# Performance work log

Hardware: AMD Instinct MI355X
Metric: run time of the kernel (lower is better)

The kernel has to match this reference:

```python
import jax, jax.numpy as jnp
import numpy as np

N = 100000
E = 1600000
IN_DIM = 128
HID = 128
OUT_DIM = 64
ORDER = 4


def setup_inputs() -> dict:
    key = jax.random.key(0)
    ks = jax.random.split(key, 10)
    x = jax.random.normal(ks[0], (N, IN_DIM), dtype=jnp.float32)
    edge_index = jax.random.randint(ks[1], (2, E), 0, N, dtype=jnp.int64)
    gen_edge_index = jax.random.randint(ks[2], (2, E), 0, N, dtype=jnp.int64)
    s = 1.0 / np.sqrt(IN_DIM)
    w_orig = jax.random.normal(ks[3], (ORDER + 1, IN_DIM, HID), dtype=jnp.float32) * s
    b_orig = jax.random.normal(ks[4], (ORDER + 1, HID), dtype=jnp.float32) * s
    w_aug = jax.random.normal(ks[5], (ORDER + 1, IN_DIM, HID), dtype=jnp.float32) * s
    b_aug = jax.random.normal(ks[6], (ORDER + 1, HID), dtype=jnp.float32) * s
    fusion_weight = jnp.ones((2,), dtype=jnp.float32)
    clf_w = jax.random.normal(ks[7], (HID, OUT_DIM), dtype=jnp.float32) / np.sqrt(HID)
    clf_b = jax.random.normal(ks[8], (OUT_DIM,), dtype=jnp.float32) / np.sqrt(HID)
    return {"x": x, "edge_index": edge_index, "gen_edge_index": gen_edge_index,
            "w_orig": w_orig, "b_orig": b_orig, "w_aug": w_aug, "b_aug": b_aug,
            "fusion_weight": fusion_weight, "clf_w": clf_w, "clf_b": clf_b}


def _beta_wavelet(x, edge_index, W, b, num_nodes):
    # add self loops
    loop = jnp.arange(num_nodes, dtype=edge_index.dtype)
    row = jnp.concatenate([edge_index[0], loop])
    col = jnp.concatenate([edge_index[1], loop])
    # symmetric normalization D^{-1/2} A D^{-1/2}
    deg = jax.ops.segment_sum(jnp.ones_like(col, dtype=x.dtype), col, num_segments=num_nodes)
    dinv = jnp.where(deg > 0, deg ** -0.5, 0.0)
    norm = dinv[row] * dinv[col]  # [E+N]
    out = x @ W[0] + b[0]
    Tx = x
    for i in range(1, ORDER + 1):
        msg = norm[:, None] * Tx[row]                      # gather + scale [E+N, D]
        Tx = jax.ops.segment_sum(msg, col, num_segments=num_nodes)  # scatter_add
        out = out + Tx @ W[i] + b[i]
    return jax.nn.relu(out)


def reference(x, edge_index, gen_edge_index, w_orig, b_orig, w_aug, b_aug, fusion_weight, clf_w, clf_b):
    num_nodes = x.shape[0]
    h_orig = _beta_wavelet(x, edge_index, w_orig, b_orig, num_nodes)
    h_aug = _beta_wavelet(x, gen_edge_index, w_aug, b_aug, num_nodes)
    w = jax.nn.softmax(fusion_weight)
    h_final = w[0] * h_orig + w[1] * h_aug
    return h_final @ clf_w + clf_b
```

## Files before the change

### kernel.cpp

```cpp
#include <hip/hip_runtime.h>

#define N_NODES 100000
#define NPAD    100096
#define NE      1600000
#define DIM     128
#define ODIM    64
#define NORDER  4
#define KTOT    640
#define NB      391
#define PB_EDGES 16384
#define PB_BLKS  98

typedef _Float16 h8 __attribute__((ext_vector_type(8)));
typedef float f4 __attribute__((ext_vector_type(4)));

__device__ __forceinline__ float2 up2(unsigned p) {
    union { unsigned u; _Float16 h[2]; } c; c.u = p;
    return make_float2((float)c.h[0], (float)c.h[1]);
}
__device__ __forceinline__ unsigned pk2(float x, float y) {
    union { unsigned u; _Float16 h[2]; } c;
    c.h[0] = (_Float16)x; c.h[1] = (_Float16)y;
    return c.u;
}
__device__ __forceinline__ unsigned short f2hbits(float x) {
    union { _Float16 h; unsigned short s; } c;
    c.h = (_Float16)x;
    return c.s;
}
__device__ __forceinline__ float h2f(unsigned short s) {
    union { unsigned short u; _Float16 h; } c;
    c.u = s;
    return (float)c.h;
}
__device__ __forceinline__ void async_cp16(const void* g, void* l) {
    __builtin_amdgcn_global_load_lds((const __attribute__((address_space(1))) void*)g,
                                     (__attribute__((address_space(3))) void*)l, 16, 0, 0);
}

__global__ __launch_bounds__(256) void hist_edges(const int* __restrict__ e0,
                                                  const int* __restrict__ e1,
                                                  int* __restrict__ bhist) {
    __shared__ int lh[NB];
    int t = threadIdx.x;
    int g = blockIdx.x >= 782;
    int blk = g ? (blockIdx.x - 782) : blockIdx.x;
    const int* colp = (g ? e1 : e0) + NE;
    int* bh = bhist + g * NB;
    for (int i = t; i < NB; i += 256) lh[i] = 0;
    __syncthreads();
    int base = blk * 2048 + t;
#pragma unroll
    for (int j = 0; j < 8; ++j) {
        int e = base + j * 256;
        if (e < NE) atomicAdd(&lh[colp[e] >> 8], 1);
    }
    __syncthreads();
    for (int i = t; i < NB; i += 256) if (lh[i]) atomicAdd(&bh[i], lh[i]);
}

__global__ void wave_scan(const int* __restrict__ in,
                          int* __restrict__ oexcl,
                          int* __restrict__ ocur,
                          int n) {
    int wv = threadIdx.x >> 6, lane = threadIdx.x & 63;
    if (wv >= 2) return;
    const int* I = in + wv * n;
    int* O = oexcl + wv * (n + 1);
    int* C = ocur + wv * n;
    int carry = 0;
    for (int base = 0; base < n; base += 64) {
        int i = base + lane;
        int v = (i < n) ? I[i] : 0;
        int s = v;
#pragma unroll
        for (int off = 1; off < 64; off <<= 1) {
            int x = __shfl_up(s, off, 64);
            if (lane >= off) s += x;
        }
        int excl = carry + s - v;
        if (i < n) {
            O[i] = excl;
            C[i] = excl;
        }
        carry += __shfl(s, 63, 64);
    }
    if (lane == 0) O[n] = carry;
}

__global__ __launch_bounds__(1024) void part_edges(const int* __restrict__ e0,
                                                   const int* __restrict__ e1,
                                                   int* __restrict__ bcursor,
                                                   unsigned* __restrict__ pairs) {
    __shared__ int lh[NB];
    __shared__ int lpos[NB];
    int t = threadIdx.x;
    int g = blockIdx.x >= PB_BLKS;
    int blk = g ? (blockIdx.x - PB_BLKS) : blockIdx.x;
    const int* rowp = (g ? e1 : e0);
    const int* colp = rowp + NE;
    int* bc = bcursor + g * NB;
    unsigned* pr = pairs + (size_t)g * NE;
    for (int i = t; i < NB; i += 1024) lh[i] = 0;
    __syncthreads();
    int base = blk * PB_EDGES + t;
    int rank[16];
    short bk[16];
    unsigned char lcv[16];
#pragma unroll
    for (int j = 0; j < 16; ++j) {
        int e = base + j * 1024;
        rank[j] = -1;
        if (e < NE) {
            int c = colp[e];
            bk[j] = (short)(c >> 8);
            lcv[j] = (unsigned char)(c & 255);
            rank[j] = atomicAdd(&lh[c >> 8], 1);
        }
    }
    __syncthreads();
    for (int i = t; i < NB; i += 1024) {
        int n = lh[i];
        lpos[i] = n ? atomicAdd(&bc[i], n) : 0;
    }
    __syncthreads();
#pragma unroll
    for (int j = 0; j < 16; ++j) {
        int e = base + j * 1024;
        if (e < NE) {
            int b = bk[j];
            pr[lpos[b] + rank[j]] = ((unsigned)rowp[e] << 8) | lcv[j];
        }
    }
}

__global__ __launch_bounds__(256) void bucket_csr(const unsigned* __restrict__ pairs,
                                                  const int* __restrict__ boff,
                                                  int* __restrict__ ptrv,
                                                  float* __restrict__ dinv,
                                                  int* __restrict__ srcv) {
    __shared__ int lcnt[256];
    __shared__ int lbase[256];
    int t = threadIdx.x;
    int g = blockIdx.x >= NB;
    int b = g ? (blockIdx.x - NB) : blockIdx.x;
    const unsigned* pr = pairs + (size_t)g * NE;
    const int* bo = boff + g * (NB + 1);
    int* pv = ptrv + g * (N_NODES + 1);
    float* dv = dinv + g * N_NODES;
    int* sv = srcv + (size_t)g * NE;
    lcnt[t] = 0;
    __syncthreads();
    int s = bo[b], e = bo[b + 1];
    for (int i = s + t; i < e; i += 256)
        atomicAdd(&lcnt[pr[i] & 255u], 1);
    __syncthreads();
    int v = lcnt[t];
    lbase[t] = v;
    __syncthreads();
    for (int off = 1; off < 256; off <<= 1) {
        int x = (t >= off) ? lbase[t - off] : 0;
        __syncthreads();
        lbase[t] += x;
        __syncthreads();
    }
    int node = (b << 8) + t;
    int gbase = s + lbase[t] - v;
    lbase[t] = gbase;
    lcnt[t] = 0;
    if (node < N_NODES) {
        pv[node] = gbase;
        dv[node] = rsqrtf((float)(v + 1));
    }
    if (b == 0 && g == 0 && t == 0) ptrv[N_NODES] = NE;
    if (b == 0 && g == 1 && t == 0) ptrv[2 * N_NODES + 1] = NE;
    __syncthreads();
    for (int i = s + t; i < e; i += 256) {
        unsigned pk = pr[i];
        int lc = (int)(pk & 255u);
        int pos = lbase[lc] + atomicAdd(&lcnt[lc], 1);
        sv[pos] = (int)(pk >> 8);
    }
}

__global__ __launch_bounds__(256) void xcast(const float* __restrict__ x,
                                             unsigned* __restrict__ Tbig) {
    int idx = blockIdx.x * 256 + threadIdx.x;
    if (idx >= NPAD * 64) return;
    int m = idx >> 6, u = idx & 63;
    int e = (m << 7) + u * 2;
    float a = (m < N_NODES) ? x[e]     : 0.f;
    float b = (m < N_NODES) ? x[e + 1] : 0.f;
    Tbig[m * 320 + u] = pk2(a, b);
}

__global__ __launch_bounds__(256) void wcast(const float* __restrict__ Wo,
                                             const float* __restrict__ Wa,
                                             const float* __restrict__ cw,
                                             unsigned short* __restrict__ Wt) {
    int idx = blockIdx.x * 256 + threadIdx.x;
    if (idx >= 2 * 5 * DIM * DIM + ODIM * DIM) return;
    if (idx < 2 * 5 * DIM * DIM) {
        int g   = idx / (5 * DIM * DIM);
        int rem = idx % (5 * DIM * DIM);
        int i   = rem / (DIM * DIM);
        int r2  = rem % (DIM * DIM);
        int k8  = r2 >> 10;
        int n   = (r2 >> 3) & 127;
        int k7  = r2 & 7;
        int k   = k8 * 8 + k7;
        const float* W = g ? Wa : Wo;
        Wt[idx] = f2hbits(W[(i * DIM + k) * DIM + n]);
    } else {
        int j = idx - 2 * 5 * DIM * DIM;
        int n = j >> 7, k = j & 127;
        Wt[idx] = f2hbits(cw[k * ODIM + n]);
    }
}

__global__ __launch_bounds__(256) void propagate(const unsigned* __restrict__ Tin,
                                                 unsigned* __restrict__ Tout,
                                                 const int* __restrict__ ptrv,
                                                 const int* __restrict__ srcv,
                                                 const float* __restrict__ dinv) {
    int gid  = blockIdx.x * 256 + threadIdx.x;
    int lane = threadIdx.x & 63;
    int v    = __builtin_amdgcn_readfirstlane(gid >> 6);
    if (v >= N_NODES) return;
    float dv = dinv[v];
    float2 self = up2(Tin[v * 320 + lane]);
    float ax = dv * dv * self.x;
    float ay = dv * dv * self.y;
    int beg = ptrv[v], end = ptrv[v + 1];
    int k = beg;
    for (; k + 16 <= end; k += 16) {
        int u[16];
#pragma unroll
        for (int j = 0; j < 16; ++j) u[j] = srcv[k + j];
        float2 tt[16];
#pragma unroll
        for (int j = 0; j < 16; ++j) tt[j] = up2(Tin[u[j] * 320 + lane]);
        float w[16];
#pragma unroll
        for (int j = 0; j < 16; ++j) w[j] = dinv[u[j]] * dv;
#pragma unroll
        for (int j = 0; j < 16; ++j) { ax += w[j] * tt[j].x; ay += w[j] * tt[j].y; }
    }
    for (; k + 4 <= end; k += 4) {
        int u[4];
#pragma unroll
        for (int j = 0; j < 4; ++j) u[j] = srcv[k + j];
        float2 tt[4];
#pragma unroll
        for (int j = 0; j < 4; ++j) tt[j] = up2(Tin[u[j] * 320 + lane]);
        float w[4];
#pragma unroll
        for (int j = 0; j < 4; ++j) w[j] = dinv[u[j]] * dv;
#pragma unroll
        for (int j = 0; j < 4; ++j) { ax += w[j] * tt[j].x; ay += w[j] * tt[j].y; }
    }
    for (; k < end; ++k) {
        int u = srcv[k];
        float w = dinv[u] * dv;
        float2 t = up2(Tin[u * 320 + lane]);
        ax += w * t.x; ay += w * t.y;
    }
    Tout[v * 320 + lane] = pk2(ax, ay);
}

__global__ __launch_bounds__(256, 3) void gemmH0(
        const unsigned short* __restrict__ A,
        const unsigned short* __restrict__ Wt,
        const float* __restrict__ bO,
        const float* __restrict__ fw,
        unsigned short* __restrict__ H0) {
    __shared__ unsigned short Bl[DIM * DIM];
    __shared__ float bsl[DIM];
    int t = threadIdx.x;
    int lane = t & 63, wv = t >> 6;
    int m0 = blockIdx.x * 128 + wv * 32;
    int l15 = lane & 15, q = lane >> 4;
    if (t < 128) {
        float s = 0.f;
        for (int i = 0; i <= NORDER; ++i) s += bO[i * DIM + t];
        bsl[t] = s;
    }
    float f0 = fw[0], f1 = fw[1];
    float mx = fmaxf(f0, f1);
    float e0 = expf(f0 - mx), e1 = expf(f1 - mx);
    float sw0 = e0 / (e0 + e1);

    f4 acc[2][8];
#pragma unroll
    for (int mt = 0; mt < 2; ++mt)
#pragma unroll
        for (int nt = 0; nt < 8; ++nt) acc[mt][nt] = (f4)(0.f);

#pragma unroll
    for (int i = 0; i < 5; ++i) {
        const unsigned short* WtI = Wt + (size_t)i * DIM * DIM;
        h8 af[2][4];
#pragma unroll
        for (int mt = 0; mt < 2; ++mt)
#pragma unroll
            for (int kc = 0; kc < 4; ++kc)
                af[mt][kc] = *(const h8*)(A + (size_t)(m0 + mt * 16 + l15) * KTOT
                                            + i * DIM + (kc * 4 + q) * 8);
#pragma unroll
        for (int c = 0; c < 8; ++c) {
            int ci = c * 4 + wv;
            async_cp16(WtI + ci * 512 + lane * 8, &Bl[ci * 512]);
        }
        __syncthreads();
#pragma unroll
        for (int kc = 0; kc < 4; ++kc) {
            int c = kc * 4 + q;
#pragma unroll
            for (int nt = 0; nt < 8; ++nt) {
                h8 bf = *(const h8*)&Bl[(size_t)(c * 128 + nt * 16 + l15) * 8];
                acc[0][nt] = __builtin_amdgcn_mfma_f32_16x16x32_f16(af[0][kc], bf, acc[0][nt], 0, 0, 0);
                acc[1][nt] = __builtin_amdgcn_mfma_f32_16x16x32_f16(af[1][kc], bf, acc[1][nt], 0, 0, 0);
            }
        }
        __syncthreads();
    }
#pragma unroll
    for (int mt = 0; mt < 2; ++mt)
#pragma unroll
        for (int nt = 0; nt < 8; ++nt) {
            float bsv = bsl[nt * 16 + l15];
#pragma unroll
            for (int r = 0; r < 4; ++r) {
                int row = m0 + mt * 16 + q * 4 + r;
                H0[(size_t)row * DIM + nt * 16 + l15] =
                    f2hbits(sw0 * fmaxf(acc[mt][nt][r] + bsv, 0.f));
            }
        }
}

__global__ __launch_bounds__(256, 2) void gemm_fused2(
        const unsigned short* __restrict__ A,
        const unsigned short* __restrict__ Wt,
        const unsigned short* __restrict__ H0,
        const float* __restrict__ bA,
        const float* __restrict__ fw,
        const unsigned short* __restrict__ clfWt,
        const float* __restrict__ clfB,
        float* __restrict__ out) {
    __shared__ unsigned short BlH[DIM * 132];
    __shared__ float bsl[DIM];
    unsigned short* Bl = BlH;
    unsigned short* Hl = BlH;
    int t = threadIdx.x;
    int lane = t & 63, wv = t >> 6;
    int m0 = blockIdx.x * 128 + wv * 32;
    int l15 = lane & 15, q = lane >> 4;
    if (t < 128) {
        float s = 0.f;
        for (int i = 0; i <= NORDER; ++i) s += bA[i * DIM + t];
        bsl[t] = s;
    }
    float f0 = fw[0], f1 = fw[1];
    float mx = fmaxf(f0, f1);
    float e0 = expf(f0 - mx), e1 = expf(f1 - mx);
    float sw1 = e1 / (e0 + e1);

    f4 acc[2][8];
#pragma unroll
    for (int mt = 0; mt < 2; ++mt)
#pragma unroll
        for (int nt = 0; nt < 8; ++nt) acc[mt][nt] = (f4)(0.f);

#pragma unroll
    for (int i = 0; i < 5; ++i) {
        const unsigned short* WtI = Wt + (size_t)i * DIM * DIM;
        h8 af[2][4];
#pragma unroll
        for (int mt = 0; mt < 2; ++mt)
#pragma unroll
            for (int kc = 0; kc < 4; ++kc)
                af[mt][kc] = *(const h8*)(A + (size_t)(m0 + mt * 16 + l15) * KTOT
                                            + i * DIM + (kc * 4 + q) * 8);
#pragma unroll
        for (int c = 0; c < 8; ++c) {
            int ci = c * 4 + wv;
            async_cp16(WtI + ci * 512 + lane * 8, &Bl[ci * 512]);
        }
        __syncthreads();
#pragma unroll
        for (int kc = 0; kc < 4; ++kc) {
            int c = kc * 4 + q;
#pragma unroll
            for (int nt = 0; nt < 8; ++nt) {
                h8 bf = *(const h8*)&Bl[(size_t)(c * 128 + nt * 16 + l15) * 8];
                acc[0][nt] = __builtin_amdgcn_mfma_f32_16x16x32_f16(af[0][kc], bf, acc[0][nt], 0, 0, 0);
                acc[1][nt] = __builtin_amdgcn_mfma_f32_16x16x32_f16(af[1][kc], bf, acc[1][nt], 0, 0, 0);
            }
        }
        __syncthreads();
    }

#pragma unroll
    for (int mt = 0; mt < 2; ++mt)
#pragma unroll
        for (int nt = 0; nt < 8; ++nt) {
            float bsv = bsl[nt * 16 + l15];
            int col = nt * 16 + l15;
#pragma unroll
            for (int r = 0; r < 4; ++r) {
                int lrow = wv * 32 + mt * 16 + q * 4 + r;
                int grow = m0 + mt * 16 + q * 4 + r;
                float h = sw1 * fmaxf(acc[mt][nt][r] + bsv, 0.f)
                        + h2f(H0[(size_t)grow * DIM + col]);
                Hl[lrow * 132 + col] = f2hbits(h);
            }
        }
    __syncthreads();

    f4 o[2][4];
#pragma unroll
    for (int mt = 0; mt < 2; ++mt)
#pragma unroll
        for (int n2 = 0; n2 < 4; ++n2) o[mt][n2] = (f4)(0.f);
#pragma unroll
    for (int kc = 0; kc < 4; ++kc) {
        int c = kc * 4 + q;
        h8 ha[2];
#pragma unroll
        for (int mt = 0; mt < 2; ++mt)
            ha[mt] = *(const h8*)&Hl[(wv * 32 + mt * 16 + l15) * 132 + c * 8];
#pragma unroll
        for (int n2 = 0; n2 < 4; ++n2) {
            h8 bf = *(const h8*)&clfWt[(size_t)(n2 * 16 + l15) * DIM + c * 8];
            o[0][n2] = __builtin_amdgcn_mfma_f32_16x16x32_f16(ha[0], bf, o[0][n2], 0, 0, 0);
            o[1][n2] = __builtin_amdgcn_mfma_f32_16x16x32_f16(ha[1], bf, o[1][n2], 0, 0, 0);
        }
    }
#pragma unroll
    for (int mt = 0; mt < 2; ++mt)
#pragma unroll
        for (int n2 = 0; n2 < 4; ++n2) {
            int col = n2 * 16 + l15;
            float cbv = clfB[col];
#pragma unroll
            for (int r = 0; r < 4; ++r) {
                int row = m0 + mt * 16 + q * 4 + r;
                if (row < N_NODES) out[(size_t)row * ODIM + col] = o[mt][n2][r] + cbv;
            }
        }
}

extern "C" void kernel_launch(void* const* d_in, const int* in_sizes, int n_in,
                              void* d_out, int out_size, void* d_ws, size_t ws_size,
                              hipStream_t stream) {
    const float* x   = (const float*)d_in[0];
    const int*   ei  = (const int*)d_in[1];
    const int*   gi  = (const int*)d_in[2];
    const float* w_o = (const float*)d_in[3];
    const float* b_o = (const float*)d_in[4];
    const float* w_a = (const float*)d_in[5];
    const float* b_a = (const float*)d_in[6];
    const float* fw  = (const float*)d_in[7];
    const float* cw  = (const float*)d_in[8];
    const float* cb  = (const float*)d_in[9];
    float* out = (float*)d_out;

    char* p = (char*)d_ws;
    auto alloc = [&](size_t bytes) {
        void* r = (void*)p;
        p += (bytes + 255) & ~(size_t)255;
        return r;
    };
    unsigned* Tbig = (unsigned*)alloc((size_t)NPAD * 320 * 4);
    unsigned short* H0 = (unsigned short*)alloc((size_t)NPAD * DIM * 2);
    unsigned short* Wt = (unsigned short*)alloc(((size_t)2 * 5 * DIM * DIM + ODIM * DIM) * 2);
    float* dinv  = (float*)alloc((size_t)2 * N_NODES * 4);
    unsigned* pairs = (unsigned*)alloc((size_t)2 * NE * 4);
    int* csr_src = (int*)alloc((size_t)2 * NE * 4);
    int* csr_ptr = (int*)alloc((size_t)2 * (N_NODES + 1) * 4);
    int* bhist   = (int*)alloc((size_t)2 * NB * 4);
    int* boff    = (int*)alloc((size_t)2 * (NB + 1) * 4);
    int* bcursor = (int*)alloc((size_t)2 * NB * 4);

    const int gP  = (N_NODES * 64 + 255) / 256;
    const int gX  = (NPAD * 64 + 255) / 256;
    const int gW  = (2 * 5 * DIM * DIM + ODIM * DIM + 255) / 256;
    const int gM  = NPAD / 128;

    xcast<<<gX, 256, 0, stream>>>(x, Tbig);
    wcast<<<gW, 256, 0, stream>>>(w_o, w_a, cw, Wt);

    hipMemsetAsync(bhist, 0, (size_t)2 * NB * 4, stream);
    hist_edges<<<2 * 782, 256, 0, stream>>>(ei, gi, bhist);
    wave_scan<<<1, 128, 0, stream>>>(bhist, boff, bcursor, NB);
    part_edges<<<2 * PB_BLKS, 1024, 0, stream>>>(ei, gi, bcursor, pairs);
    bucket_csr<<<2 * NB, 256, 0, stream>>>(pairs, boff, csr_ptr, dinv, csr_src);

    for (int i = 1; i <= NORDER; ++i)
        propagate<<<gP, 256, 0, stream>>>(Tbig + (i - 1) * 64, Tbig + i * 64,
                                          csr_ptr, csr_src, dinv);
    gemmH0<<<gM, 256, 0, stream>>>((const unsigned short*)Tbig, Wt, b_o, fw, H0);

    {
        const int* pv = csr_ptr + (N_NODES + 1);
        const int* sv = csr_src + (size_t)NE;
        const float* dv = dinv + (size_t)N_NODES;
        for (int i = 1; i <= NORDER; ++i)
            propagate<<<gP, 256, 0, stream>>>(Tbig + (i - 1) * 64, Tbig + i * 64,
                                              pv, sv, dv);
    }
    gemm_fused2<<<gM, 256, 0, stream>>>((const unsigned short*)Tbig,
                                        Wt + (size_t)5 * DIM * DIM,
                                        H0, b_a, fw,
                                        Wt + (size_t)2 * 5 * DIM * DIM, cb, out);
}
```

Before: 812.2 us.

## Propagate degree-prescaled features to drop per-edge dinv gathers

Propagation now works on S = D^{-1/2}·T. Each step becomes a plain neighbour sum scaled by 1/deg of the destination node, so the random per-edge dinv[u] load and multiply disappear. The initial features are prescaled by dinv in a new cast kernel, and the GEMM epilogues undo the scaling per row with 1/dinv before adding the bias. The edge loop is also collapsed into a single 16-wide loop whose tail slots are padded with a zeroed dummy node, which removes the remainder loops at the cost of some wasted gathers. The feature buffer layout changes to a 256-element row stride, with X held in separate buffers.

Result: faster. 783.4 us (-3.6%).

```diff
diff --git a/kernel.cpp b/kernel.cpp
--- a/kernel.cpp
+++ b/kernel.cpp
@@ -6,7 +6,6 @@
 #define DIM     128
 #define ODIM    64
 #define NORDER  4
-#define KTOT    640
 #define NB      391
 #define PB_EDGES 16384
 #define PB_BLKS  98
@@ -183,15 +182,24 @@
     }
 }
 
-__global__ __launch_bounds__(256) void xcast(const float* __restrict__ x,
-                                             unsigned* __restrict__ Tbig) {
+__global__ __launch_bounds__(256) void s0cast(const float* __restrict__ x,
+                                              const float* __restrict__ dinv,
+                                              unsigned* __restrict__ S0o,
+                                              unsigned* __restrict__ S0a) {
     int idx = blockIdx.x * 256 + threadIdx.x;
     if (idx >= NPAD * 64) return;
     int m = idx >> 6, u = idx & 63;
-    int e = (m << 7) + u * 2;
-    float a = (m < N_NODES) ? x[e]     : 0.f;
-    float b = (m < N_NODES) ? x[e + 1] : 0.f;
-    Tbig[m * 320 + u] = pk2(a, b);
+    if (m < N_NODES) {
+        int e = (m << 7) + u * 2;
+        float a = x[e], b = x[e + 1];
+        float d0 = dinv[m];
+        float d1 = dinv[N_NODES + m];
+        S0o[idx] = pk2(d0 * a, d0 * b);
+        S0a[idx] = pk2(d1 * a, d1 * b);
+    } else {
+        S0o[idx] = 0u;
+        S0a[idx] = 0u;
+    }
 }
 
 __global__ __launch_bounds__(256) void wcast(const float* __restrict__ Wo,
@@ -218,6 +226,7 @@
     }
 }
 
+template<int SIN>
 __global__ __launch_bounds__(256) void propagate(const unsigned* __restrict__ Tin,
                                                  unsigned* __restrict__ Tout,
                                                  const int* __restrict__ ptrv,
@@ -228,50 +237,37 @@
     int v    = __builtin_amdgcn_readfirstlane(gid >> 6);
     if (v >= N_NODES) return;
     float dv = dinv[v];
-    float2 self = up2(Tin[v * 320 + lane]);
-    float ax = dv * dv * self.x;
-    float ay = dv * dv * self.y;
+    float2 self = up2(Tin[(size_t)v * SIN + lane]);
+    float ax = self.x, ay = self.y;
     int beg = ptrv[v], end = ptrv[v + 1];
-    int k = beg;
-    for (; k + 16 <= end; k += 16) {
+    for (int k = beg; k < end; k += 16) {
         int u[16];
 #pragma unroll
-        for (int j = 0; j < 16; ++j) u[j] = srcv[k + j];
-        float2 tt[16];
-#pragma unroll
-        for (int j = 0; j < 16; ++j) tt[j] = up2(Tin[u[j] * 320 + lane]);
-        float w[16];
-#pragma unroll
-        for (int j = 0; j < 16; ++j) w[j] = dinv[u[j]] * dv;
-#pragma unroll
-        for (int j = 0; j < 16; ++j) { ax += w[j] * tt[j].x; ay += w[j] * tt[j].y; }
-    }
-    for (; k + 4 <= end; k += 4) {
-        int u[4];
-#pragma unroll
-        for (int j = 0; j < 4; ++j) u[j] = srcv[k + j];
-        float2 tt[4];
-#pragma unroll
-        for (int j = 0; j < 4; ++j) tt[j] = up2(Tin[u[j] * 320 + lane]);
-        float w[4];
-#pragma unroll
-        for (int j = 0; j < 4; ++j) w[j] = dinv[u[j]] * dv;
-#pragma unroll
-        for (int j = 0; j < 4; ++j) { ax += w[j] * tt[j].x; ay += w[j] * tt[j].y; }
-    }
-    for (; k < end; ++k) {
-        int u = srcv[k];
-        float w = dinv[u] * dv;
-        float2 t = up2(Tin[u * 320 + lane]);
-        ax += w * t.x; ay += w * t.y;
-    }
-    Tout[v * 320 + lane] = pk2(ax, ay);
+        for (int j = 0; j < 16; ++j) {
+            int e  = k + j;
+            int su = srcv[e < NE ? e : (NE - 1)];
+            u[j]   = (e < end) ? su : N_NODES;
+        }
+        unsigned tw[16];
+#pragma unroll
+        for (int j = 0; j < 16; ++j)
+            tw[j] = Tin[(size_t)((unsigned)u[j] * SIN) + lane];
+#pragma unroll
+        for (int j = 0; j < 16; ++j) {
+            float2 t = up2(tw[j]);
+            ax += t.x; ay += t.y;
+        }
+    }
+    float s2 = dv * dv;
+    Tout[(size_t)v * 256 + lane] = pk2(s2 * ax, s2 * ay);
 }
 
 __global__ __launch_bounds__(256, 3) void gemmH0(
+        const unsigned short* __restrict__ A0,
         const unsigned short* __restrict__ A,
         const unsigned short* __restrict__ Wt,
         const float* __restrict__ bO,
+        const float* __restrict__ dinv,
         const float* __restrict__ fw,
         unsigned short* __restrict__ H0) {
     __shared__ unsigned short Bl[DIM * DIM];
@@ -299,13 +295,15 @@
 #pragma unroll
     for (int i = 0; i < 5; ++i) {
         const unsigned short* WtI = Wt + (size_t)i * DIM * DIM;
+        const unsigned short* Ai = (i == 0) ? A0 : (A + (size_t)(i - 1) * DIM);
+        const int rs = (i == 0) ? DIM : 512;
         h8 af[2][4];
 #pragma unroll
         for (int mt = 0; mt < 2; ++mt)
 #pragma unroll
             for (int kc = 0; kc < 4; ++kc)
-                af[mt][kc] = *(const h8*)(A + (size_t)(m0 + mt * 16 + l15) * KTOT
-                                            + i * DIM + (kc * 4 + q) * 8);
+                af[mt][kc] = *(const h8*)(Ai + (size_t)(m0 + mt * 16 + l15) * rs
+                                             + (kc * 4 + q) * 8);
 #pragma unroll
         for (int c = 0; c < 8; ++c) {
             int ci = c * 4 + wv;
@@ -325,7 +323,13 @@
         __syncthreads();
     }
 #pragma unroll
-    for (int mt = 0; mt < 2; ++mt)
+    for (int mt = 0; mt < 2; ++mt) {
+        float rd[4];
+#pragma unroll
+        for (int r = 0; r < 4; ++r) {
+            int row = m0 + mt * 16 + q * 4 + r;
+            rd[r] = 1.0f / dinv[row < N_NODES ? row : (N_NODES - 1)];
+        }
 #pragma unroll
         for (int nt = 0; nt < 8; ++nt) {
             float bsv = bsl[nt * 16 + l15];
@@ -333,16 +337,19 @@
             for (int r = 0; r < 4; ++r) {
                 int row = m0 + mt * 16 + q * 4 + r;
                 H0[(size_t)row * DIM + nt * 16 + l15] =
-                    f2hbits(sw0 * fmaxf(acc[mt][nt][r] + bsv, 0.f));
+                    f2hbits(sw0 * fmaxf(rd[r] * acc[mt][nt][r] + bsv, 0.f));
             }
         }
+    }
 }
 
 __global__ __launch_bounds__(256, 2) void gemm_fused2(
+        const unsigned short* __restrict__ A0,
         const unsigned short* __restrict__ A,
         const unsigned short* __restrict__ Wt,
         const unsigned short* __restrict__ H0,
         const float* __restrict__ bA,
+        const float* __restrict__ dinv,
         const float* __restrict__ fw,
         const unsigned short* __restrict__ clfWt,
         const float* __restrict__ clfB,
@@ -374,13 +381,15 @@
 #pragma unroll
     for (int i = 0; i < 5; ++i) {
         const unsigned short* WtI = Wt + (size_t)i * DIM * DIM;
+        const unsigned short* Ai = (i == 0) ? A0 : (A + (size_t)(i - 1) * DIM);
+        const int rs = (i == 0) ? DIM : 512;
         h8 af[2][4];
 #pragma unroll
         for (int mt = 0; mt < 2; ++mt)
 #pragma unroll
             for (int kc = 0; kc < 4; ++kc)
-                af[mt][kc] = *(const h8*)(A + (size_t)(m0 + mt * 16 + l15) * KTOT
-                                            + i * DIM + (kc * 4 + q) * 8);
+                af[mt][kc] = *(const h8*)(Ai + (size_t)(m0 + mt * 16 + l15) * rs
+                                             + (kc * 4 + q) * 8);
 #pragma unroll
         for (int c = 0; c < 8; ++c) {
             int ci = c * 4 + wv;
@@ -401,7 +410,13 @@
     }
 
 #pragma unroll
-    for (int mt = 0; mt < 2; ++mt)
+    for (int mt = 0; mt < 2; ++mt) {
+        float rd[4];
+#pragma unroll
+        for (int r = 0; r < 4; ++r) {
+            int row = m0 + mt * 16 + q * 4 + r;
+            rd[r] = 1.0f / dinv[row < N_NODES ? row : (N_NODES - 1)];
+        }
 #pragma unroll
         for (int nt = 0; nt < 8; ++nt) {
             float bsv = bsl[nt * 16 + l15];
@@ -410,11 +425,12 @@
             for (int r = 0; r < 4; ++r) {
                 int lrow = wv * 32 + mt * 16 + q * 4 + r;
                 int grow = m0 + mt * 16 + q * 4 + r;
-                float h = sw1 * fmaxf(acc[mt][nt][r] + bsv, 0.f)
+                float h = sw1 * fmaxf(rd[r] * acc[mt][nt][r] + bsv, 0.f)
                         + h2f(H0[(size_t)grow * DIM + col]);
                 Hl[lrow * 132 + col] = f2hbits(h);
             }
         }
+    }
     __syncthreads();
 
     f4 o[2][4];
@@ -471,7 +487,9 @@
         p += (bytes + 255) & ~(size_t)255;
         return r;
     };
-    unsigned* Tbig = (unsigned*)alloc((size_t)NPAD * 320 * 4);
+    unsigned* Tbig = (unsigned*)alloc((size_t)NPAD * 256 * 4);
+    unsigned* S0o  = (unsigned*)alloc((size_t)NPAD * 64 * 4);
+    unsigned* S0a  = (unsigned*)alloc((size_t)NPAD * 64 * 4);
     unsigned short* H0 = (unsigned short*)alloc((size_t)NPAD * DIM * 2);
     unsigned short* Wt = (unsigned short*)alloc(((size_t)2 * 5 * DIM * DIM + ODIM * DIM) * 2);
     float* dinv  = (float*)alloc((size_t)2 * N_NODES * 4);
@@ -487,30 +505,38 @@
     const int gW  = (2 * 5 * DIM * DIM + ODIM * DIM + 255) / 256;
     const int gM  = NPAD / 128;
 
-    xcast<<<gX, 256, 0, stream>>>(x, Tbig);
+    hipMemsetAsync(Tbig + (size_t)N_NODES * 256, 0,
+                   (size_t)(NPAD - N_NODES) * 256 * 4, stream);
+    hipMemsetAsync(bhist, 0, (size_t)2 * NB * 4, stream);
+
     wcast<<<gW, 256, 0, stream>>>(w_o, w_a, cw, Wt);
 
-    hipMemsetAsync(bhist, 0, (size_t)2 * NB * 4, stream);
     hist_edges<<<2 * 782, 256, 0, stream>>>(ei, gi, bhist);
     wave_scan<<<1, 128, 0, stream>>>(bhist, boff, bcursor, NB);
     part_edges<<<2 * PB_BLKS, 1024, 0, stream>>>(ei, gi, bcursor, pairs);
     bucket_csr<<<2 * NB, 256, 0, stream>>>(pairs, boff, csr_ptr, dinv, csr_src);
 
-    for (int i = 1; i <= NORDER; ++i)
-        propagate<<<gP, 256, 0, stream>>>(Tbig + (i - 1) * 64, Tbig + i * 64,
-                                          csr_ptr, csr_src, dinv);
-    gemmH0<<<gM, 256, 0, stream>>>((const unsigned short*)Tbig, Wt, b_o, fw, H0);
+    s0cast<<<gX, 256, 0, stream>>>(x, dinv, S0o, S0a);
+
+    propagate<64><<<gP, 256, 0, stream>>>(S0o, Tbig, csr_ptr, csr_src, dinv);
+    propagate<256><<<gP, 256, 0, stream>>>(Tbig, Tbig + 64, csr_ptr, csr_src, dinv);
+    propagate<256><<<gP, 256, 0, stream>>>(Tbig + 64, Tbig + 128, csr_ptr, csr_src, dinv);
+    propagate<256><<<gP, 256, 0, stream>>>(Tbig + 128, Tbig + 192, csr_ptr, csr_src, dinv);
+    gemmH0<<<gM, 256, 0, stream>>>((const unsigned short*)S0o, (const unsigned short*)Tbig,
+                                   Wt, b_o, dinv, fw, H0);
 
     {
         const int* pv = csr_ptr + (N_NODES + 1);
         const int* sv = csr_src + (size_t)NE;
         const float* dv = dinv + (size_t)N_NODES;
-        for (int i = 1; i <= NORDER; ++i)
-            propagate<<<gP, 256, 0, stream>>>(Tbig + (i - 1) * 64, Tbig + i * 64,
-                                              pv, sv, dv);
-    }
-    gemm_fused2<<<gM, 256, 0, stream>>>((const unsigned short*)Tbig,
+        propagate<64><<<gP, 256, 0, stream>>>(S0a, Tbig, pv, sv, dv);
+        propagate<256><<<gP, 256, 0, stream>>>(Tbig, Tbig + 64, pv, sv, dv);
+        propagate<256><<<gP, 256, 0, stream>>>(Tbig + 64, Tbig + 128, pv, sv, dv);
+        propagate<256><<<gP, 256, 0, stream>>>(Tbig + 128, Tbig + 192, pv, sv, dv);
+    }
+    gemm_fused2<<<gM, 256, 0, stream>>>((const unsigned short*)S0a,
+                                        (const unsigned short*)Tbig,
                                         Wt + (size_t)5 * DIM * DIM,
-                                        H0, b_a, fw,
+                                        H0, b_a, dinv + N_NODES, fw,
                                         Wt + (size_t)2 * 5 * DIM * DIM, cb, out);
 }
```
